# Optimization experiments

Measured on AMD Instinct MI355X. Metric: run time of the kernel, lower is better.

Reference implementation:

```python
import jax, jax.numpy as jnp
import numpy as np

N, E = 16384, 262144
D_NODE, D_EDGE, H = 256, 64, 8
EPS = 1e-5

def _lin(key, din, dout):
    kw, kb = jax.random.split(key)
    s = 1.0 / np.sqrt(din)
    W = jax.random.uniform(kw, (din, dout), jnp.float32, -s, s)
    b = jax.random.uniform(kb, (dout,), jnp.float32, -s, s)
    return W, b

def setup_inputs() -> dict:
    key = jax.random.key(0)
    ks = jax.random.split(key, 12)
    node_features = jax.random.normal(ks[0], (N, D_NODE), jnp.float32)
    edge_index = jax.random.randint(ks[1], (2, E), 0, N, jnp.int64)
    edge_features = jax.random.normal(ks[2], (E, D_EDGE), jnp.float32)
    Wn, bn = _lin(ks[3], D_NODE, D_NODE)
    Wq, bq = _lin(ks[4], D_NODE, D_NODE)
    Wk, bk = _lin(ks[5], D_NODE, D_NODE)
    Wv, bv = _lin(ks[6], D_NODE, D_NODE)
    We, be = _lin(ks[7], D_EDGE, D_NODE)
    A1, a1 = _lin(ks[8], 3 * D_NODE, D_NODE)
    A2, a2 = _lin(ks[9], D_NODE, H)
    gamma = jnp.ones((D_NODE,), jnp.float32)
    beta = jnp.zeros((D_NODE,), jnp.float32)
    return dict(node_features=node_features, edge_index=edge_index,
                edge_features=edge_features, Wn=Wn, bn=bn, Wq=Wq, bq=bq,
                Wk=Wk, bk=bk, Wv=Wv, bv=bv, We=We, be=be,
                A1=A1, a1=a1, A2=A2, a2=a2, gamma=gamma, beta=beta)

def _leaky(x):
    return jnp.where(x > 0, x, 0.2 * x)

def reference(node_features, edge_index, edge_features, Wn, bn, Wq, bq,
              Wk, bk, Wv, bv, We, be, A1, a1, A2, a2, gamma, beta):
    h = node_features @ Wn + bn                      # [N, d]
    q = node_features @ Wq + bq
    k = node_features @ Wk + bk
    v = node_features @ Wv + bv
    edge_h = edge_features @ We + be                 # [E, d]
    src, tgt = edge_index[0], edge_index[1]
    attn_in = jnp.concatenate([q[src], k[tgt], edge_h], axis=-1)  # [E, 3d]
    scores = _leaky(_leaky(attn_in @ A1 + a1) @ A2 + a2)          # [E, H]
    # softmax over ALL edges (dim=0) of head-mean, as in the original
    w = jax.nn.softmax(scores.mean(axis=-1), axis=0)              # [E]
    out = jnp.zeros_like(node_features).at[src].add(w[:, None] * v[tgt])
    x = h + out                                      # dropout is identity (eval)
    mu = x.mean(-1, keepdims=True)
    var = ((x - mu) ** 2).mean(-1, keepdims=True)
    return (x - mu) / jnp.sqrt(var + EPS) * gamma + beta
```

## Files before the change

kernel.cpp:

```cpp
#include <hip/hip_runtime.h>
#include <stdint.h>

#define NN 16384
#define EE 262144
#define DD 256

typedef float f32x4 __attribute__((ext_vector_type(4)));
typedef short s16x8 __attribute__((ext_vector_type(8)));
typedef unsigned short u16x4 __attribute__((ext_vector_type(4)));
typedef unsigned short u16x8 __attribute__((ext_vector_type(8)));

#define AS1 __attribute__((address_space(1)))
#define AS3 __attribute__((address_space(3)))

__device__ __forceinline__ float bf2f(unsigned short u) {
  union { unsigned int i; float f; } v; v.i = ((unsigned int)u) << 16; return v.f;
}
__device__ __forceinline__ unsigned short f2bf(float f) {
  union { float f; unsigned int i; } v; v.f = f;
  unsigned int r = v.i + 0x7fffu + ((v.i >> 16) & 1u);
  return (unsigned short)(r >> 16);
}
__device__ __forceinline__ float lrelu(float x) { return x > 0.f ? x : 0.2f * x; }

__global__ __launch_bounds__(256) void prep_kernel(
    const float* __restrict__ Wn, const float* __restrict__ bn,
    const float* __restrict__ Wq, const float* __restrict__ bq,
    const float* __restrict__ Wk, const float* __restrict__ bk,
    const float* __restrict__ Wv, const float* __restrict__ bv,
    const float* __restrict__ We, const float* __restrict__ be,
    const float* __restrict__ A1, const float* __restrict__ a1,
    unsigned short* __restrict__ BcatT, float* __restrict__ bcat,
    unsigned short* __restrict__ WeaT, float* __restrict__ bcomb)
{
  const int b = blockIdx.x, t = threadIdx.x;
  if (b < 256) {
    float acc = 0.f;
    for (int j = 0; j < 256; ++j) acc += Wq[b * 256 + j] * A1[j * 256 + t];
    BcatT[(512 + t) * 256 + b] = f2bf(acc);
  } else if (b < 512) {
    int k = b - 256; float acc = 0.f;
    for (int j = 0; j < 256; ++j) acc += Wk[k * 256 + j] * A1[(256 + j) * 256 + t];
    BcatT[(768 + t) * 256 + k] = f2bf(acc);
  } else if (b < 576) {
    int k = b - 512; float acc = 0.f;
    for (int j = 0; j < 256; ++j) acc += We[k * 256 + j] * A1[(512 + j) * 256 + t];
    WeaT[t * 64 + k] = f2bf(acc);
  } else if (b == 576) {
    float acc = a1[t];
    for (int j = 0; j < 256; ++j) {
      acc += bq[j] * A1[j * 256 + t];
      acc += bk[j] * A1[(256 + j) * 256 + t];
      acc += be[j] * A1[(512 + j) * 256 + t];
    }
    bcomb[t] = acc;
  } else if (b < 705) {
    int b2 = b - 577;
    for (int rr = 0; rr < 4; ++rr) {
      int np = b2 * 4 + rr;
      float v = (np < 256) ? Wn[t * 256 + np] : Wv[t * 256 + (np - 256)];
      BcatT[np * 256 + t] = f2bf(v);
    }
  } else {
    bcat[t] = bn[t];
    bcat[256 + t] = bv[t];
    bcat[512 + t] = 0.f;
    bcat[768 + t] = 0.f;
  }
}

__global__ __launch_bounds__(256) void conv_bf16_kernel(
    const float* __restrict__ in, unsigned short* __restrict__ o)
{
  size_t i = (size_t)blockIdx.x * 256 + threadIdx.x;
  const f32x4* p = (const f32x4*)(in + i * 8);
  f32x4 a = p[0], b = p[1];
  u16x8 r = { f2bf(a[0]), f2bf(a[1]), f2bf(a[2]), f2bf(a[3]),
              f2bf(b[0]), f2bf(b[1]), f2bf(b[2]), f2bf(b[3]) };
  *(u16x8*)(o + i * 8) = r;
}

__global__ __launch_bounds__(256, 1) void node_gemm_kernel(
    const unsigned short* __restrict__ Abf,
    const unsigned short* __restrict__ BT,
    const float* __restrict__ bias,
    float* __restrict__ hout, unsigned short* __restrict__ vout,
    unsigned short* __restrict__ Qa, unsigned short* __restrict__ Ka)
{
  __shared__ __align__(16) unsigned short Al[128 * 64];
  __shared__ __align__(16) unsigned short Bl[128 * 64];
  const int t = threadIdx.x;
  const int wid = t >> 6, lane = t & 63;
  const int quad = lane >> 4, l15 = lane & 15;
  const int mblk = blockIdx.x & 127, nblk = blockIdx.x >> 7;
  const int m0 = mblk * 128, n0 = nblk * 128;
  const int mh = wid >> 1, nh = wid & 1;
  const int srow = lane >> 3, sslot = lane & 7;

  f32x4 acc[4][4];
  #pragma unroll
  for (int i = 0; i < 4; ++i)
    #pragma unroll
    for (int j = 0; j < 4; ++j) acc[i][j] = (f32x4){0.f, 0.f, 0.f, 0.f};

  for (int ks = 0; ks < 4; ++ks) {
    const int k0 = ks * 64;
    #pragma unroll
    for (int j = 0; j < 4; ++j) {
      int cj = wid * 4 + j;
      int row = cj * 8 + srow;
      const unsigned short* ga =
          Abf + (size_t)(m0 + row) * 256 + k0 + ((sslot ^ (row & 7)) * 8);
      __builtin_amdgcn_global_load_lds((AS1 const void*)ga,
                                       (AS3 void*)(Al + cj * 512), 16, 0, 0);
      const unsigned short* gb =
          BT + (size_t)(n0 + row) * 256 + k0 + ((sslot ^ (row & 7)) * 8);
      __builtin_amdgcn_global_load_lds((AS1 const void*)gb,
                                       (AS3 void*)(Bl + cj * 512), 16, 0, 0);
    }
    __syncthreads();
    s16x8 af[4][2], bfr[4][2];
    #pragma unroll
    for (int mt = 0; mt < 4; ++mt) {
      int row = mh * 64 + mt * 16 + l15;
      #pragma unroll
      for (int kk = 0; kk < 2; ++kk) {
        int s = (kk * 4 + quad) ^ (row & 7);
        af[mt][kk] = *(const s16x8*)(Al + row * 64 + s * 8);
      }
    }
    #pragma unroll
    for (int nt = 0; nt < 4; ++nt) {
      int row = nh * 64 + nt * 16 + l15;
      #pragma unroll
      for (int kk = 0; kk < 2; ++kk) {
        int s = (kk * 4 + quad) ^ (row & 7);
        bfr[nt][kk] = *(const s16x8*)(Bl + row * 64 + s * 8);
      }
    }
    #pragma unroll
    for (int mt = 0; mt < 4; ++mt)
      #pragma unroll
      for (int nt = 0; nt < 4; ++nt) {
        acc[mt][nt] = __builtin_amdgcn_mfma_f32_16x16x32_bf16(
            af[mt][0], bfr[nt][0], acc[mt][nt], 0, 0, 0);
        acc[mt][nt] = __builtin_amdgcn_mfma_f32_16x16x32_bf16(
            af[mt][1], bfr[nt][1], acc[mt][nt], 0, 0, 0);
      }
    __syncthreads();
  }

  #pragma unroll
  for (int nt = 0; nt < 4; ++nt) {
    int n = n0 + nh * 64 + nt * 16 + l15;
    float bb = bias[n];
    int seg = n >> 8;
    int ncol = n & 255;
    #pragma unroll
    for (int mt = 0; mt < 4; ++mt) {
      int m = m0 + mh * 64 + mt * 16 + quad * 4;
      f32x4 a = acc[mt][nt];
      #pragma unroll
      for (int r = 0; r < 4; ++r) {
        float val = a[r] + bb;
        size_t idx = (size_t)(m + r) * 256 + ncol;
        if (seg == 0) hout[idx] = val;
        else if (seg == 1) vout[idx] = f2bf(val);
        else if (seg == 2) Qa[idx] = f2bf(val);
        else Ka[idx] = f2bf(val);
      }
    }
  }
}

__global__ __launch_bounds__(256, 1) void edge_scores_kernel(
    const int* __restrict__ eidx, const float* __restrict__ ef,
    const unsigned short* __restrict__ Qa, const unsigned short* __restrict__ Ka,
    const unsigned short* __restrict__ WeaT, const float* __restrict__ bcomb,
    const float* __restrict__ A2, const float* __restrict__ a2g,
    float* __restrict__ P, float* __restrict__ Z, int* __restrict__ deg)
{
  __shared__ __align__(16) unsigned short efl[64 * 64];
  __shared__ __align__(16) float A2l[256 * 12];
  __shared__ __align__(16) float pl[4 * 64 * 8];
  __shared__ int srcl[64], tgtl[64];
  const int t = threadIdx.x;
  const int wid = t >> 6, lane = t & 63, quad = lane >> 4, l15 = lane & 15;
  const int eb = blockIdx.x * 64;

  {
    const f32x4* sp = (const f32x4*)(A2 + t * 8);
    f32x4 x0 = sp[0], x1 = sp[1];
    *(f32x4*)&A2l[t * 12] = x0;
    *(f32x4*)&A2l[t * 12 + 4] = x1;
  }
  if (t < 64) { int s_ = eidx[eb + t]; srcl[t] = s_; atomicAdd(&deg[s_], 1); }
  else if (t < 128) { tgtl[t - 64] = eidx[EE + eb + (t - 64)]; }
  {
    int r = t >> 2, q4 = t & 3;
    const f32x4* sp = (const f32x4*)(ef + (size_t)(eb + r) * 64 + q4 * 16);
    f32x4 v0 = sp[0], v1 = sp[1], v2 = sp[2], v3 = sp[3];
    u16x8 w0 = { f2bf(v0[0]), f2bf(v0[1]), f2bf(v0[2]), f2bf(v0[3]),
                 f2bf(v1[0]), f2bf(v1[1]), f2bf(v1[2]), f2bf(v1[3]) };
    u16x8 w1 = { f2bf(v2[0]), f2bf(v2[1]), f2bf(v2[2]), f2bf(v2[3]),
                 f2bf(v3[0]), f2bf(v3[1]), f2bf(v3[2]), f2bf(v3[3]) };
    int s0_ = (2 * q4) ^ (r & 7), s1_ = (2 * q4 + 1) ^ (r & 7);
    *(u16x8*)&efl[r * 64 + s0_ * 8] = w0;
    *(u16x8*)&efl[r * 64 + s1_ * 8] = w1;
  }
  s16x8 af[4][2];
  f32x4 bc[4];
  #pragma unroll
  for (int ct = 0; ct < 4; ++ct) {
    int ch = wid * 64 + ct * 16 + l15;
    af[ct][0] = *(const s16x8*)(WeaT + ch * 64 + quad * 8);
    af[ct][1] = *(const s16x8*)(WeaT + ch * 64 + 32 + quad * 8);
    bc[ct] = *(const f32x4*)(bcomb + wid * 64 + ct * 16 + quad * 4);
  }
  __syncthreads();

  f32x4 acc[4][4];
  #pragma unroll
  for (int i = 0; i < 4; ++i)
    #pragma unroll
    for (int j = 0; j < 4; ++j) acc[i][j] = (f32x4){0.f, 0.f, 0.f, 0.f};

  #pragma unroll
  for (int et = 0; et < 4; ++et) {
    int e = et * 16 + l15;
    s16x8 b0 = *(const s16x8*)(efl + e * 64 + ((quad ^ (e & 7)) * 8));
    s16x8 b1 = *(const s16x8*)(efl + e * 64 + (((4 + quad) ^ (e & 7)) * 8));
    #pragma unroll
    for (int ct = 0; ct < 4; ++ct) {
      acc[ct][et] = __builtin_amdgcn_mfma_f32_16x16x32_bf16(af[ct][0], b0, acc[ct][et], 0, 0, 0);
      acc[ct][et] = __builtin_amdgcn_mfma_f32_16x16x32_bf16(af[ct][1], b1, acc[ct][et], 0, 0, 0);
    }
  }
  #pragma unroll
  for (int et = 0; et < 4; ++et) {
    int e = et * 16 + l15;
    int se = srcl[e], te = tgtl[e];
    #pragma unroll
    for (int ct = 0; ct < 4; ++ct) {
      u16x4 qv = *(const u16x4*)(Qa + (size_t)se * 256 + wid * 64 + ct * 16 + quad * 4);
      u16x4 kv = *(const u16x4*)(Ka + (size_t)te * 256 + wid * 64 + ct * 16 + quad * 4);
      f32x4 x = acc[ct][et];
      #pragma unroll
      for (int r = 0; r < 4; ++r) {
        float xv = x[r] + bf2f(qv[r]) + bf2f(kv[r]) + bc[ct][r];
        x[r] = lrelu(xv);
      }
      acc[ct][et] = x;
    }
  }
  float part[4][8];
  #pragma unroll
  for (int i = 0; i < 4; ++i)
    #pragma unroll
    for (int j = 0; j < 8; ++j) part[i][j] = 0.f;
  #pragma unroll
  for (int ct = 0; ct < 4; ++ct) {
    int chb = wid * 64 + ct * 16 + quad * 4;
    #pragma unroll
    for (int r = 0; r < 4; ++r) {
      f32x4 w0 = *(const f32x4*)&A2l[(chb + r) * 12];
      f32x4 w1 = *(const f32x4*)&A2l[(chb + r) * 12 + 4];
      #pragma unroll
      for (int et = 0; et < 4; ++et) {
        float m = acc[ct][et][r];
        part[et][0] += m * w0[0]; part[et][1] += m * w0[1];
        part[et][2] += m * w0[2]; part[et][3] += m * w0[3];
        part[et][4] += m * w1[0]; part[et][5] += m * w1[1];
        part[et][6] += m * w1[2]; part[et][7] += m * w1[3];
      }
    }
  }
  #pragma unroll
  for (int et = 0; et < 4; ++et)
    #pragma unroll
    for (int hh = 0; hh < 8; ++hh) {
      part[et][hh] += __shfl_xor(part[et][hh], 16);
      part[et][hh] += __shfl_xor(part[et][hh], 32);
    }
  if (quad == 0) {
    #pragma unroll
    for (int et = 0; et < 4; ++et) {
      f32x4 p0 = { part[et][0], part[et][1], part[et][2], part[et][3] };
      f32x4 p1 = { part[et][4], part[et][5], part[et][6], part[et][7] };
      int e = et * 16 + l15;
      *(f32x4*)&pl[(wid * 64 + e) * 8] = p0;
      *(f32x4*)&pl[(wid * 64 + e) * 8 + 4] = p1;
    }
  }
  __syncthreads();
  if (t < 64) {
    float tot[8] = {0.f, 0.f, 0.f, 0.f, 0.f, 0.f, 0.f, 0.f};
    #pragma unroll
    for (int w2 = 0; w2 < 4; ++w2)
      #pragma unroll
      for (int hh = 0; hh < 8; ++hh) tot[hh] += pl[(w2 * 64 + t) * 8 + hh];
    float sacc = 0.f;
    #pragma unroll
    for (int hh = 0; hh < 8; ++hh) sacc += lrelu(tot[hh] + a2g[hh]);
    float p = __expf(sacc * 0.125f);
    P[eb + t] = p;
    #pragma unroll
    for (int d = 1; d < 64; d <<= 1) p += __shfl_xor(p, d);
    if (t == 0) atomicAdd(Z, p);
  }
}

__global__ __launch_bounds__(256) void scan_kernel(
    const int* __restrict__ deg, int* __restrict__ startA, int* __restrict__ cursor)
{
  __shared__ int ls[256];
  int t = threadIdx.x;
  int base = t * 64;
  int s = 0;
  for (int i = 0; i < 64; ++i) s += deg[base + i];
  ls[t] = s;
  __syncthreads();
  for (int d = 1; d < 256; d <<= 1) {
    int v = ls[t];
    if (t >= d) v += ls[t - d];
    __syncthreads();
    ls[t] = v;
    __syncthreads();
  }
  int run = ls[t] - s;
  for (int i = 0; i < 64; ++i) {
    int dv = deg[base + i];
    startA[base + i] = run;
    cursor[base + i] = run;
    run += dv;
  }
  if (t == 255) startA[NN] = run;
}

__global__ __launch_bounds__(256) void perm_kernel(
    const int* __restrict__ eidx, int* __restrict__ cursor, int* __restrict__ perm)
{
  int e = blockIdx.x * 256 + threadIdx.x;
  int s = eidx[e];
  int pos = atomicAdd(&cursor[s], 1);
  perm[pos] = e;
}

__global__ __launch_bounds__(64) void scatter_ln_kernel(
    const int* __restrict__ perm, const int* __restrict__ startA,
    const float* __restrict__ P, const float* __restrict__ Zp,
    const int* __restrict__ tgt, const unsigned short* __restrict__ vbuf,
    const float* __restrict__ hbuf, const float* __restrict__ gamma,
    const float* __restrict__ beta, float* __restrict__ out)
{
  int n = blockIdx.x, lane = threadIdx.x;
  float invZ = 1.f / Zp[0];
  int s0 = startA[n], s1 = startA[n + 1];
  float a0 = 0.f, a1_ = 0.f, a2_ = 0.f, a3_ = 0.f;
  for (int i = s0; i < s1; ++i) {
    int e = perm[i];
    float w = P[e] * invZ;
    int te = tgt[e];
    u16x4 vv = *(const u16x4*)(vbuf + (size_t)te * 256 + lane * 4);
    a0 += w * bf2f(vv[0]); a1_ += w * bf2f(vv[1]);
    a2_ += w * bf2f(vv[2]); a3_ += w * bf2f(vv[3]);
  }
  f32x4 hv = *(const f32x4*)(hbuf + (size_t)n * 256 + lane * 4);
  float x0 = hv[0] + a0, x1 = hv[1] + a1_, x2 = hv[2] + a2_, x3 = hv[3] + a3_;
  float sum = x0 + x1 + x2 + x3;
  float sq = x0 * x0 + x1 * x1 + x2 * x2 + x3 * x3;
  #pragma unroll
  for (int d = 1; d < 64; d <<= 1) { sum += __shfl_xor(sum, d); sq += __shfl_xor(sq, d); }
  float mu = sum * (1.f / 256.f);
  float var = sq * (1.f / 256.f) - mu * mu;
  float rstd = rsqrtf(var + 1e-5f);
  f32x4 g = *(const f32x4*)(gamma + lane * 4);
  f32x4 b = *(const f32x4*)(beta + lane * 4);
  f32x4 o;
  o[0] = (x0 - mu) * rstd * g[0] + b[0];
  o[1] = (x1 - mu) * rstd * g[1] + b[1];
  o[2] = (x2 - mu) * rstd * g[2] + b[2];
  o[3] = (x3 - mu) * rstd * g[3] + b[3];
  *(f32x4*)(out + (size_t)n * 256 + lane * 4) = o;
}

extern "C" void kernel_launch(void* const* d_in, const int* in_sizes, int n_in,
                              void* d_out, int out_size, void* d_ws, size_t ws_size,
                              hipStream_t stream)
{
  (void)in_sizes; (void)n_in; (void)out_size; (void)ws_size;
  const float* nf    = (const float*)d_in[0];
  const int*   eidx  = (const int*)  d_in[1];
  const float* ef    = (const float*)d_in[2];
  const float* Wn    = (const float*)d_in[3];
  const float* bn    = (const float*)d_in[4];
  const float* Wq    = (const float*)d_in[5];
  const float* bq    = (const float*)d_in[6];
  const float* Wk    = (const float*)d_in[7];
  const float* bk    = (const float*)d_in[8];
  const float* Wv    = (const float*)d_in[9];
  const float* bv    = (const float*)d_in[10];
  const float* We    = (const float*)d_in[11];
  const float* be    = (const float*)d_in[12];
  const float* A1    = (const float*)d_in[13];
  const float* a1    = (const float*)d_in[14];
  const float* A2    = (const float*)d_in[15];
  const float* a2    = (const float*)d_in[16];
  const float* gamma = (const float*)d_in[17];
  const float* beta  = (const float*)d_in[18];
  float* out = (float*)d_out;

  char* ws = (char*)d_ws;
  size_t off = 0;
  auto take = [&](size_t bytes) {
    size_t r = off; off += (bytes + 255) & ~(size_t)255; return r;
  };
  float* Z       = (float*)(ws + take(16));
  int*   deg     = (int*)  (ws + take((size_t)NN * 4));
  int*   startA  = (int*)  (ws + take((size_t)(NN + 1) * 4));
  int*   cursor  = (int*)  (ws + take((size_t)NN * 4));
  int*   perm    = (int*)  (ws + take((size_t)EE * 4));
  float* P       = (float*)(ws + take((size_t)EE * 4));
  float* hbuf    = (float*)(ws + take((size_t)NN * DD * 4));
  unsigned short* vbuf  = (unsigned short*)(ws + take((size_t)NN * DD * 2));
  unsigned short* QaB   = (unsigned short*)(ws + take((size_t)NN * DD * 2));
  unsigned short* KaB   = (unsigned short*)(ws + take((size_t)NN * DD * 2));
  unsigned short* BcatT = (unsigned short*)(ws + take((size_t)1024 * 256 * 2));
  float* bcat    = (float*)(ws + take(1024 * 4));
  unsigned short* WeaT  = (unsigned short*)(ws + take((size_t)256 * 64 * 2));
  float* bcomb   = (float*)(ws + take(256 * 4));
  unsigned short* nfb   = (unsigned short*)(ws + take((size_t)NN * DD * 2));

  hipMemsetAsync(d_ws, 0, 256 + (size_t)NN * 4, stream);

  prep_kernel<<<706, 256, 0, stream>>>(Wn, bn, Wq, bq, Wk, bk, Wv, bv,
                                       We, be, A1, a1, BcatT, bcat, WeaT, bcomb);
  conv_bf16_kernel<<<(NN * DD / 8) / 256, 256, 0, stream>>>(nf, nfb);
  node_gemm_kernel<<<1024, 256, 0, stream>>>(nfb, BcatT, bcat, hbuf, vbuf, QaB, KaB);
  edge_scores_kernel<<<EE / 64, 256, 0, stream>>>(eidx, ef, QaB, KaB, WeaT,
                                                  bcomb, A2, a2, P, Z, deg);
  scan_kernel<<<1, 256, 0, stream>>>(deg, startA, cursor);
  perm_kernel<<<EE / 256, 256, 0, stream>>>(eidx, cursor, perm);
  scatter_ln_kernel<<<NN, 64, 0, stream>>>(perm, startA, P, Z, eidx + EE,
                                           vbuf, hbuf, gamma, beta, out);
}
```

Baseline: 372.4 us.

## Sort edges by source before scoring, write scores in CSR order

The degree histogram moves into the bf16 conversion kernel, and the scan and permutation now run before edge scoring. This lets the edge-scores kernel process edges in source-sorted order, storing src, tgt and P already permuted, so the scatter/layernorm kernel reads contiguously with no perm indirection. The edge kernel now starts its accumulators from the gathered Q+K values using 16-byte loads, enabled by a channel permutation applied to WeaT, bcomb and A2. It also raises occupancy to 4 blocks per SM and packs 4 nodes per block in the scatter kernel. The cost is a scattered gather of edge features through perm, plus extra src/tgt arrays.

```diff
diff --git a/kernel.cpp b/kernel.cpp
--- a/kernel.cpp
+++ b/kernel.cpp
@@ -22,6 +22,12 @@
   return (unsigned short)(r >> 16);
 }
 __device__ __forceinline__ float lrelu(float x) { return x > 0.f ? x : 0.2f * x; }
+
+__device__ __forceinline__ int chanperm(int c) {
+  int hi = c & ~63, loc = c & 63;
+  int ct = loc >> 4, quad = (loc >> 2) & 3, r = loc & 3;
+  return hi | (quad * 16 + ct * 4 + r);
+}
 
 __global__ __launch_bounds__(256) void prep_kernel(
     const float* __restrict__ Wn, const float* __restrict__ bn,
@@ -30,8 +36,10 @@
     const float* __restrict__ Wv, const float* __restrict__ bv,
     const float* __restrict__ We, const float* __restrict__ be,
     const float* __restrict__ A1, const float* __restrict__ a1,
+    const float* __restrict__ A2,
     unsigned short* __restrict__ BcatT, float* __restrict__ bcat,
-    unsigned short* __restrict__ WeaT, float* __restrict__ bcomb)
+    unsigned short* __restrict__ WeaT, float* __restrict__ bcomb,
+    float* __restrict__ A2p)
 {
   const int b = blockIdx.x, t = threadIdx.x;
   if (b < 256) {
@@ -45,7 +53,7 @@
   } else if (b < 576) {
     int k = b - 512; float acc = 0.f;
     for (int j = 0; j < 256; ++j) acc += We[k * 256 + j] * A1[(512 + j) * 256 + t];
-    WeaT[t * 64 + k] = f2bf(acc);
+    WeaT[chanperm(t) * 64 + k] = f2bf(acc);
   } else if (b == 576) {
     float acc = a1[t];
     for (int j = 0; j < 256; ++j) {
@@ -53,7 +61,7 @@
       acc += bk[j] * A1[(256 + j) * 256 + t];
       acc += be[j] * A1[(512 + j) * 256 + t];
     }
-    bcomb[t] = acc;
+    bcomb[chanperm(t)] = acc;
   } else if (b < 705) {
     int b2 = b - 577;
     for (int rr = 0; rr < 4; ++rr) {
@@ -61,16 +69,20 @@
       float v = (np < 256) ? Wn[t * 256 + np] : Wv[t * 256 + (np - 256)];
       BcatT[np * 256 + t] = f2bf(v);
     }
-  } else {
+  } else if (b == 705) {
     bcat[t] = bn[t];
     bcat[256 + t] = bv[t];
     bcat[512 + t] = 0.f;
     bcat[768 + t] = 0.f;
-  }
-}
-
-__global__ __launch_bounds__(256) void conv_bf16_kernel(
-    const float* __restrict__ in, unsigned short* __restrict__ o)
+  } else {
+    int m = chanperm(t);
+    for (int j = 0; j < 8; ++j) A2p[m * 8 + j] = A2[t * 8 + j];
+  }
+}
+
+__global__ __launch_bounds__(256) void conv_hist_kernel(
+    const float* __restrict__ in, unsigned short* __restrict__ o,
+    const int* __restrict__ eidx, int* __restrict__ deg)
 {
   size_t i = (size_t)blockIdx.x * 256 + threadIdx.x;
   const f32x4* p = (const f32x4*)(in + i * 8);
@@ -78,6 +90,10 @@
   u16x8 r = { f2bf(a[0]), f2bf(a[1]), f2bf(a[2]), f2bf(a[3]),
               f2bf(b[0]), f2bf(b[1]), f2bf(b[2]), f2bf(b[3]) };
   *(u16x8*)(o + i * 8) = r;
+  if (blockIdx.x < EE / 256) {
+    int e = blockIdx.x * 256 + threadIdx.x;
+    atomicAdd(&deg[eidx[e]], 1);
+  }
 }
 
 __global__ __launch_bounds__(256, 1) void node_gemm_kernel(
@@ -173,32 +189,83 @@
   }
 }
 
-__global__ __launch_bounds__(256, 1) void edge_scores_kernel(
-    const int* __restrict__ eidx, const float* __restrict__ ef,
+__global__ __launch_bounds__(256) void scan_kernel(
+    const int* __restrict__ deg, int* __restrict__ startA, int* __restrict__ cursor)
+{
+  __shared__ int ls[256];
+  const int t = threadIdx.x;
+  int4 d[16];
+  int s = 0;
+  #pragma unroll
+  for (int i = 0; i < 16; ++i) {
+    d[i] = ((const int4*)deg)[t * 16 + i];
+    s += d[i].x + d[i].y + d[i].z + d[i].w;
+  }
+  ls[t] = s;
+  __syncthreads();
+  for (int dd = 1; dd < 256; dd <<= 1) {
+    int v = ls[t];
+    if (t >= dd) v += ls[t - dd];
+    __syncthreads();
+    ls[t] = v;
+    __syncthreads();
+  }
+  int run = ls[t] - s;
+  #pragma unroll
+  for (int i = 0; i < 16; ++i) {
+    int4 o;
+    o.x = run; run += d[i].x;
+    o.y = run; run += d[i].y;
+    o.z = run; run += d[i].z;
+    o.w = run; run += d[i].w;
+    ((int4*)startA)[t * 16 + i] = o;
+    ((int4*)cursor)[t * 16 + i] = o;
+  }
+  if (t == 255) startA[NN] = run;
+}
+
+__global__ __launch_bounds__(256) void perm_kernel(
+    const int* __restrict__ eidx, int* __restrict__ cursor,
+    int* __restrict__ perm, int* __restrict__ srcp, int* __restrict__ tgtp)
+{
+  int e = blockIdx.x * 256 + threadIdx.x;
+  int s = eidx[e], tg = eidx[EE + e];
+  int pos = atomicAdd(&cursor[s], 1);
+  perm[pos] = e;
+  srcp[pos] = s;
+  tgtp[pos] = tg;
+}
+
+__global__ __launch_bounds__(256, 4) void edge_scores_kernel(
+    const int* __restrict__ perm, const int* __restrict__ srcp,
+    const int* __restrict__ tgtp, const float* __restrict__ ef,
     const unsigned short* __restrict__ Qa, const unsigned short* __restrict__ Ka,
     const unsigned short* __restrict__ WeaT, const float* __restrict__ bcomb,
-    const float* __restrict__ A2, const float* __restrict__ a2g,
-    float* __restrict__ P, float* __restrict__ Z, int* __restrict__ deg)
+    const float* __restrict__ A2p, const float* __restrict__ a2g,
+    float* __restrict__ Pp, float* __restrict__ Z)
 {
   __shared__ __align__(16) unsigned short efl[64 * 64];
   __shared__ __align__(16) float A2l[256 * 12];
   __shared__ __align__(16) float pl[4 * 64 * 8];
+  __shared__ __align__(16) float bcl[256];
   __shared__ int srcl[64], tgtl[64];
   const int t = threadIdx.x;
   const int wid = t >> 6, lane = t & 63, quad = lane >> 4, l15 = lane & 15;
   const int eb = blockIdx.x * 64;
 
   {
-    const f32x4* sp = (const f32x4*)(A2 + t * 8);
+    const f32x4* sp = (const f32x4*)(A2p + t * 8);
     f32x4 x0 = sp[0], x1 = sp[1];
     *(f32x4*)&A2l[t * 12] = x0;
     *(f32x4*)&A2l[t * 12 + 4] = x1;
   }
-  if (t < 64) { int s_ = eidx[eb + t]; srcl[t] = s_; atomicAdd(&deg[s_], 1); }
-  else if (t < 128) { tgtl[t - 64] = eidx[EE + eb + (t - 64)]; }
+  if (t < 64) srcl[t] = srcp[eb + t];
+  else if (t < 128) tgtl[t - 64] = tgtp[eb + (t - 64)];
+  else if (t < 192) ((f32x4*)bcl)[t - 128] = ((const f32x4*)bcomb)[t - 128];
   {
     int r = t >> 2, q4 = t & 3;
-    const f32x4* sp = (const f32x4*)(ef + (size_t)(eb + r) * 64 + q4 * 16);
+    int pe = perm[eb + r];
+    const f32x4* sp = (const f32x4*)(ef + (size_t)pe * 64 + q4 * 16);
     f32x4 v0 = sp[0], v1 = sp[1], v2 = sp[2], v3 = sp[3];
     u16x8 w0 = { f2bf(v0[0]), f2bf(v0[1]), f2bf(v0[2]), f2bf(v0[3]),
                  f2bf(v1[0]), f2bf(v1[1]), f2bf(v1[2]), f2bf(v1[3]) };
@@ -208,51 +275,57 @@
     *(u16x8*)&efl[r * 64 + s0_ * 8] = w0;
     *(u16x8*)&efl[r * 64 + s1_ * 8] = w1;
   }
-  s16x8 af[4][2];
-  f32x4 bc[4];
-  #pragma unroll
-  for (int ct = 0; ct < 4; ++ct) {
-    int ch = wid * 64 + ct * 16 + l15;
-    af[ct][0] = *(const s16x8*)(WeaT + ch * 64 + quad * 8);
-    af[ct][1] = *(const s16x8*)(WeaT + ch * 64 + 32 + quad * 8);
-    bc[ct] = *(const f32x4*)(bcomb + wid * 64 + ct * 16 + quad * 4);
-  }
   __syncthreads();
 
   f32x4 acc[4][4];
-  #pragma unroll
-  for (int i = 0; i < 4; ++i)
-    #pragma unroll
-    for (int j = 0; j < 4; ++j) acc[i][j] = (f32x4){0.f, 0.f, 0.f, 0.f};
-
-  #pragma unroll
-  for (int et = 0; et < 4; ++et) {
-    int e = et * 16 + l15;
-    s16x8 b0 = *(const s16x8*)(efl + e * 64 + ((quad ^ (e & 7)) * 8));
-    s16x8 b1 = *(const s16x8*)(efl + e * 64 + (((4 + quad) ^ (e & 7)) * 8));
+  {
+    const int cb = wid * 64 + quad * 16;
+    #pragma unroll
+    for (int eo = 0; eo < 2; ++eo) {
+      u16x8 q0[2], q1[2], k0[2], k1[2];
+      #pragma unroll
+      for (int x = 0; x < 2; ++x) {
+        int e = (eo * 2 + x) * 16 + l15;
+        const unsigned short* qr = Qa + (size_t)srcl[e] * 256 + cb;
+        const unsigned short* kr = Ka + (size_t)tgtl[e] * 256 + cb;
+        q0[x] = *(const u16x8*)qr; q1[x] = *(const u16x8*)(qr + 8);
+        k0[x] = *(const u16x8*)kr; k1[x] = *(const u16x8*)(kr + 8);
+      }
+      #pragma unroll
+      for (int x = 0; x < 2; ++x) {
+        int et = eo * 2 + x;
+        #pragma unroll
+        for (int r = 0; r < 4; ++r) {
+          acc[0][et][r] = bf2f(q0[x][r])     + bf2f(k0[x][r]);
+          acc[1][et][r] = bf2f(q0[x][4 + r]) + bf2f(k0[x][4 + r]);
+          acc[2][et][r] = bf2f(q1[x][r])     + bf2f(k1[x][r]);
+          acc[3][et][r] = bf2f(q1[x][4 + r]) + bf2f(k1[x][4 + r]);
+        }
+      }
+    }
+  }
+
+  {
+    s16x8 af0[4], af1[4];
     #pragma unroll
     for (int ct = 0; ct < 4; ++ct) {
-      acc[ct][et] = __builtin_amdgcn_mfma_f32_16x16x32_bf16(af[ct][0], b0, acc[ct][et], 0, 0, 0);
-      acc[ct][et] = __builtin_amdgcn_mfma_f32_16x16x32_bf16(af[ct][1], b1, acc[ct][et], 0, 0, 0);
-    }
-  }
-  #pragma unroll
-  for (int et = 0; et < 4; ++et) {
-    int e = et * 16 + l15;
-    int se = srcl[e], te = tgtl[e];
-    #pragma unroll
-    for (int ct = 0; ct < 4; ++ct) {
-      u16x4 qv = *(const u16x4*)(Qa + (size_t)se * 256 + wid * 64 + ct * 16 + quad * 4);
-      u16x4 kv = *(const u16x4*)(Ka + (size_t)te * 256 + wid * 64 + ct * 16 + quad * 4);
-      f32x4 x = acc[ct][et];
-      #pragma unroll
-      for (int r = 0; r < 4; ++r) {
-        float xv = x[r] + bf2f(qv[r]) + bf2f(kv[r]) + bc[ct][r];
-        x[r] = lrelu(xv);
-      }
-      acc[ct][et] = x;
-    }
-  }
+      int ch = wid * 64 + ct * 16 + l15;
+      af0[ct] = *(const s16x8*)(WeaT + ch * 64 + quad * 8);
+      af1[ct] = *(const s16x8*)(WeaT + ch * 64 + 32 + quad * 8);
+    }
+    #pragma unroll
+    for (int et = 0; et < 4; ++et) {
+      int e = et * 16 + l15;
+      s16x8 b0 = *(const s16x8*)(efl + e * 64 + ((quad ^ (e & 7)) * 8));
+      s16x8 b1 = *(const s16x8*)(efl + e * 64 + (((4 + quad) ^ (e & 7)) * 8));
+      #pragma unroll
+      for (int ct = 0; ct < 4; ++ct) {
+        acc[ct][et] = __builtin_amdgcn_mfma_f32_16x16x32_bf16(af0[ct], b0, acc[ct][et], 0, 0, 0);
+        acc[ct][et] = __builtin_amdgcn_mfma_f32_16x16x32_bf16(af1[ct], b1, acc[ct][et], 0, 0, 0);
+      }
+    }
+  }
+
   float part[4][8];
   #pragma unroll
   for (int i = 0; i < 4; ++i)
@@ -261,13 +334,14 @@
   #pragma unroll
   for (int ct = 0; ct < 4; ++ct) {
     int chb = wid * 64 + ct * 16 + quad * 4;
+    f32x4 bc = *(const f32x4*)&bcl[chb];
     #pragma unroll
     for (int r = 0; r < 4; ++r) {
       f32x4 w0 = *(const f32x4*)&A2l[(chb + r) * 12];
       f32x4 w1 = *(const f32x4*)&A2l[(chb + r) * 12 + 4];
       #pragma unroll
       for (int et = 0; et < 4; ++et) {
-        float m = acc[ct][et][r];
+        float m = lrelu(acc[ct][et][r] + bc[r]);
         part[et][0] += m * w0[0]; part[et][1] += m * w0[1];
         part[et][2] += m * w0[2]; part[et][3] += m * w0[3];
         part[et][4] += m * w1[0]; part[et][5] += m * w1[1];
@@ -294,76 +368,56 @@
   }
   __syncthreads();
   if (t < 64) {
-    float tot[8] = {0.f, 0.f, 0.f, 0.f, 0.f, 0.f, 0.f, 0.f};
-    #pragma unroll
-    for (int w2 = 0; w2 < 4; ++w2)
-      #pragma unroll
-      for (int hh = 0; hh < 8; ++hh) tot[hh] += pl[(w2 * 64 + t) * 8 + hh];
+    f32x4 t0 = {0.f, 0.f, 0.f, 0.f}, t1 = {0.f, 0.f, 0.f, 0.f};
+    #pragma unroll
+    for (int w2 = 0; w2 < 4; ++w2) {
+      t0 += *(const f32x4*)&pl[(w2 * 64 + t) * 8];
+      t1 += *(const f32x4*)&pl[(w2 * 64 + t) * 8 + 4];
+    }
     float sacc = 0.f;
     #pragma unroll
-    for (int hh = 0; hh < 8; ++hh) sacc += lrelu(tot[hh] + a2g[hh]);
+    for (int j = 0; j < 4; ++j) {
+      sacc += lrelu(t0[j] + a2g[j]);
+      sacc += lrelu(t1[j] + a2g[4 + j]);
+    }
     float p = __expf(sacc * 0.125f);
-    P[eb + t] = p;
+    Pp[eb + t] = p;
     #pragma unroll
     for (int d = 1; d < 64; d <<= 1) p += __shfl_xor(p, d);
     if (t == 0) atomicAdd(Z, p);
   }
 }
 
-__global__ __launch_bounds__(256) void scan_kernel(
-    const int* __restrict__ deg, int* __restrict__ startA, int* __restrict__ cursor)
-{
-  __shared__ int ls[256];
-  int t = threadIdx.x;
-  int base = t * 64;
-  int s = 0;
-  for (int i = 0; i < 64; ++i) s += deg[base + i];
-  ls[t] = s;
-  __syncthreads();
-  for (int d = 1; d < 256; d <<= 1) {
-    int v = ls[t];
-    if (t >= d) v += ls[t - d];
-    __syncthreads();
-    ls[t] = v;
-    __syncthreads();
-  }
-  int run = ls[t] - s;
-  for (int i = 0; i < 64; ++i) {
-    int dv = deg[base + i];
-    startA[base + i] = run;
-    cursor[base + i] = run;
-    run += dv;
-  }
-  if (t == 255) startA[NN] = run;
-}
-
-__global__ __launch_bounds__(256) void perm_kernel(
-    const int* __restrict__ eidx, int* __restrict__ cursor, int* __restrict__ perm)
-{
-  int e = blockIdx.x * 256 + threadIdx.x;
-  int s = eidx[e];
-  int pos = atomicAdd(&cursor[s], 1);
-  perm[pos] = e;
-}
-
-__global__ __launch_bounds__(64) void scatter_ln_kernel(
-    const int* __restrict__ perm, const int* __restrict__ startA,
-    const float* __restrict__ P, const float* __restrict__ Zp,
-    const int* __restrict__ tgt, const unsigned short* __restrict__ vbuf,
-    const float* __restrict__ hbuf, const float* __restrict__ gamma,
-    const float* __restrict__ beta, float* __restrict__ out)
-{
-  int n = blockIdx.x, lane = threadIdx.x;
-  float invZ = 1.f / Zp[0];
-  int s0 = startA[n], s1 = startA[n + 1];
+__global__ __launch_bounds__(256) void scatter_ln_kernel(
+    const int* __restrict__ startA, const float* __restrict__ Pp,
+    const float* __restrict__ Zp, const int* __restrict__ tgtp,
+    const unsigned short* __restrict__ vbuf, const float* __restrict__ hbuf,
+    const float* __restrict__ gamma, const float* __restrict__ beta,
+    float* __restrict__ out)
+{
+  const int wid = threadIdx.x >> 6, lane = threadIdx.x & 63;
+  const int n = blockIdx.x * 4 + wid;
+  const float invZ = 1.f / Zp[0];
+  const int s0 = startA[n], s1 = startA[n + 1];
   float a0 = 0.f, a1_ = 0.f, a2_ = 0.f, a3_ = 0.f;
-  for (int i = s0; i < s1; ++i) {
-    int e = perm[i];
-    float w = P[e] * invZ;
-    int te = tgt[e];
-    u16x4 vv = *(const u16x4*)(vbuf + (size_t)te * 256 + lane * 4);
-    a0 += w * bf2f(vv[0]); a1_ += w * bf2f(vv[1]);
-    a2_ += w * bf2f(vv[2]); a3_ += w * bf2f(vv[3]);
+  int i = s0;
+  for (; i + 1 < s1; i += 2) {
+    float w0 = Pp[i], w1 = Pp[i + 1];
+    int t0 = tgtp[i], t1 = tgtp[i + 1];
+    u16x4 v0 = *(const u16x4*)(vbuf + (size_t)t0 * 256 + lane * 4);
+    u16x4 v1 = *(const u16x4*)(vbuf + (size_t)t1 * 256 + lane * 4);
+    w0 *= invZ; w1 *= invZ;
+    a0 += w0 * bf2f(v0[0]) + w1 * bf2f(v1[0]);
+    a1_ += w0 * bf2f(v0[1]) + w1 * bf2f(v1[1]);
+    a2_ += w0 * bf2f(v0[2]) + w1 * bf2f(v1[2]);
+    a3_ += w0 * bf2f(v0[3]) + w1 * bf2f(v1[3]);
+  }
+  if (i < s1) {
+    float w0 = Pp[i] * invZ;
+    int t0 = tgtp[i];
+    u16x4 v0 = *(const u16x4*)(vbuf + (size_t)t0 * 256 + lane * 4);
+    a0 += w0 * bf2f(v0[0]); a1_ += w0 * bf2f(v0[1]);
+    a2_ += w0 * bf2f(v0[2]); a3_ += w0 * bf2f(v0[3]);
   }
   f32x4 hv = *(const f32x4*)(hbuf + (size_t)n * 256 + lane * 4);
   float x0 = hv[0] + a0, x1 = hv[1] + a1_, x2 = hv[2] + a2_, x3 = hv[3] + a3_;
@@ -420,7 +474,9 @@
   int*   startA  = (int*)  (ws + take((size_t)(NN + 1) * 4));
   int*   cursor  = (int*)  (ws + take((size_t)NN * 4));
   int*   perm    = (int*)  (ws + take((size_t)EE * 4));
-  float* P       = (float*)(ws + take((size_t)EE * 4));
+  int*   srcp    = (int*)  (ws + take((size_t)EE * 4));
+  int*   tgtp    = (int*)  (ws + take((size_t)EE * 4));
+  float* Pp      = (float*)(ws + take((size_t)EE * 4));
   float* hbuf    = (float*)(ws + take((size_t)NN * DD * 4));
   unsigned short* vbuf  = (unsigned short*)(ws + take((size_t)NN * DD * 2));
   unsigned short* QaB   = (unsigned short*)(ws + take((size_t)NN * DD * 2));
@@ -429,18 +485,20 @@
   float* bcat    = (float*)(ws + take(1024 * 4));
   unsigned short* WeaT  = (unsigned short*)(ws + take((size_t)256 * 64 * 2));
   float* bcomb   = (float*)(ws + take(256 * 4));
+  float* A2p     = (float*)(ws + take(256 * 8 * 4));
   unsigned short* nfb   = (unsigned short*)(ws + take((size_t)NN * DD * 2));
 
   hipMemsetAsync(d_ws, 0, 256 + (size_t)NN * 4, stream);
 
-  prep_kernel<<<706, 256, 0, stream>>>(Wn, bn, Wq, bq, Wk, bk, Wv, bv,
-                                       We, be, A1, a1, BcatT, bcat, WeaT, bcomb);
-  conv_bf16_kernel<<<(NN * DD / 8) / 256, 256, 0, stream>>>(nf, nfb);
+  prep_kernel<<<707, 256, 0, stream>>>(Wn, bn, Wq, bq, Wk, bk, Wv, bv,
+                                       We, be, A1, a1, A2,
+                                       BcatT, bcat, WeaT, bcomb, A2p);
+  conv_hist_kernel<<<(NN * DD / 8) / 256, 256, 0, stream>>>(nf, nfb, eidx, deg);
   node_gemm_kernel<<<1024, 256, 0, stream>>>(nfb, BcatT, bcat, hbuf, vbuf, QaB, KaB);
-  edge_scores_kernel<<<EE / 64, 256, 0, stream>>>(eidx, ef, QaB, KaB, WeaT,
-                                                  bcomb, A2, a2, P, Z, deg);
   scan_kernel<<<1, 256, 0, stream>>>(deg, startA, cursor);
-  perm_kernel<<<EE / 256, 256, 0, stream>>>(eidx, cursor, perm);
-  scatter_ln_kernel<<<NN, 64, 0, stream>>>(perm, startA, P, Z, eidx + EE,
-                                           vbuf, hbuf, gamma, beta, out);
-}
+  perm_kernel<<<EE / 256, 256, 0, stream>>>(eidx, cursor, perm, srcp, tgtp);
+  edge_scores_kernel<<<EE / 64, 256, 0, stream>>>(perm, srcp, tgtp, ef, QaB, KaB,
+                                                  WeaT, bcomb, A2p, a2, Pp, Z);
+  scatter_ln_kernel<<<NN / 4, 256, 0, stream>>>(startA, Pp, Z, tgtp, vbuf, hbuf,
+                                                gamma, beta, out);
+}
```

After: 347.9 us. 1.07x faster.
